# Kernel optimization log

Hardware: AMD Instinct MI355X
Metric: run time of the kernel (lower is better)

Reference implementation:

```python
import jax, jax.numpy as jnp
import numpy as np

B = 65536; T = 7
N_NUM = 32; N_CAT = 16; CARD = 100; D_CAT = 16
D_STATE = 96; D_HID = 192; S_DIM = 64; DT = 1.0
D_IN = N_NUM + N_CAT * D_CAT + 8  # 296
D_Z = 3 * D_STATE + 64            # 352

def _ln(x, g, b, eps=1e-5):
    m = x.mean(-1, keepdims=True)
    v = ((x - m) ** 2).mean(-1, keepdims=True)
    return (x - m) * jax.lax.rsqrt(v + eps) * g + b

def _gelu(x):
    return jax.nn.gelu(x, approximate=False)  # matches torch F.gelu default (erf)

def _forward(x_num, x_static, cat_emb, day_emb, xproj_w, xproj_b, h0,
             bln_g, bln_b, fc1_w, fc1_b, fc2_w, fc2_b,
             spln_g, spln_b, sp1_w, sp1_b, sp2_w, sp2_b,
             base_w, base_b, hln_g, hln_b,
             hm1_w, hm1_b, hm2_w, hm2_b,
             hq1_w, hq1_b, hq2_w, hq2_b,
             hn1_w, hn1_b, hn2_w, hn2_b, x_cat):
    Bsz = x_num.shape[0]
    # categorical embeddings: per-feature table lookup -> (B,T,N_CAT,D_CAT)
    emb = jax.vmap(lambda tab, idx: tab[idx], in_axes=(0, 2), out_axes=2)(cat_emb, x_cat)
    emb = emb.reshape(Bsz, T, N_CAT * D_CAT)
    # day ids are arange(1,8), shared over batch
    day = jnp.broadcast_to(day_emb[1:8], (Bsz, T, 8))
    x = jnp.concatenate([x_num, emb, day], axis=-1)          # (B,T,D_IN)
    x = x @ xproj_w + xproj_b                                # (B,T,D_STATE)

    def step(h, xt):  # Euler-integrated LN+MLP residual cell (dropout = eval identity)
        z = jnp.concatenate([h, xt], axis=-1)                # (B,2*D_STATE)
        z = _ln(z, bln_g, bln_b)
        dh = _gelu(z @ fc1_w + fc1_b) @ fc2_w + fc2_b
        h = h + DT * dh
        return h, h

    h0b = jnp.broadcast_to(h0, (Bsz, D_STATE))
    _, hs = jax.lax.scan(step, h0b, jnp.swapaxes(x, 0, 1))   # (T,B,D_STATE)
    H = jnp.swapaxes(hs, 0, 1)                               # (B,T,D_STATE)
    h_last = H[:, -1]
    h_mean = H.mean(axis=1)
    h_max = H.max(axis=1)

    s = _ln(x_static, spln_g, spln_b)
    s64 = _gelu(s @ sp1_w + sp1_b) @ sp2_w + sp2_b           # (B,64)

    z = jnp.concatenate([h_last, h_mean, h_max, s64], axis=-1)  # (B,D_Z)
    z = _ln(z, hln_g, hln_b)
    base = x_static @ base_w + base_b                        # (B,)
    mean = base + _gelu(z @ hm1_w + hm1_b) @ hm2_w + hm2_b
    q20 = base + _gelu(z @ hq1_w + hq1_b) @ hq2_w + hq2_b
    neg_logit = _gelu(z @ hn1_w + hn1_b) @ hn2_w + hn2_b
    return mean, q20, neg_logit

def setup_inputs() -> dict:
    key = jax.random.key(0)
    ks = iter(jax.random.split(key, 64))
    def w(shape, scale=0.02):
        return (scale * jax.random.normal(next(ks), shape)).astype(jnp.float32)
    def zz(shape):
        return jnp.zeros(shape, jnp.float32)
    def oo(shape):
        return jnp.ones(shape, jnp.float32)
    inp = {
        "x_num": jax.random.normal(next(ks), (B, T, N_NUM), jnp.float32),
        "x_static": jax.random.normal(next(ks), (B, S_DIM), jnp.float32),
        "x_cat": jax.random.randint(next(ks), (B, T, N_CAT), 0, CARD),
        "cat_emb": w((N_CAT, CARD + 1, D_CAT), 1.0),
        "day_emb": w((8, 8), 1.0),
        "xproj_w": w((D_IN, D_STATE)), "xproj_b": zz((D_STATE,)),
        "h0": zz((D_STATE,)),
        "bln_g": oo((2 * D_STATE,)), "bln_b": zz((2 * D_STATE,)),
        "fc1_w": w((2 * D_STATE, D_HID)), "fc1_b": zz((D_HID,)),
        "fc2_w": w((D_HID, D_STATE)), "fc2_b": zz((D_STATE,)),
        "spln_g": oo((S_DIM,)), "spln_b": zz((S_DIM,)),
        "sp1_w": w((S_DIM, 128)), "sp1_b": zz((128,)),
        "sp2_w": w((128, 64)), "sp2_b": zz((64,)),
        "base_w": w((S_DIM,)), "base_b": zz(()),
        "hln_g": oo((D_Z,)), "hln_b": zz((D_Z,)),
        "hm1_w": w((D_Z, D_HID)), "hm1_b": zz((D_HID,)),
        "hm2_w": w((D_HID,)), "hm2_b": zz(()),
        "hq1_w": w((D_Z, D_HID)), "hq1_b": zz((D_HID,)),
        "hq2_w": w((D_HID,)), "hq2_b": zz(()),
        "hn1_w": w((D_Z, D_HID // 2)), "hn1_b": zz((D_HID // 2,)),
        "hn2_w": w((D_HID // 2,)), "hn2_b": zz(()),
    }
    return inp

def reference(x_num, x_static, x_cat, cat_emb, day_emb, xproj_w, xproj_b, h0,
              bln_g, bln_b, fc1_w, fc1_b, fc2_w, fc2_b,
              spln_g, spln_b, sp1_w, sp1_b, sp2_w, sp2_b,
              base_w, base_b, hln_g, hln_b,
              hm1_w, hm1_b, hm2_w, hm2_b,
              hq1_w, hq1_b, hq2_w, hq2_b,
              hn1_w, hn1_b, hn2_w, hn2_b):
    return _forward(x_num, x_static, cat_emb, day_emb, xproj_w, xproj_b, h0,
                    bln_g, bln_b, fc1_w, fc1_b, fc2_w, fc2_b,
                    spln_g, spln_b, sp1_w, sp1_b, sp2_w, sp2_b,
                    base_w, base_b, hln_g, hln_b,
                    hm1_w, hm1_b, hm2_w, hm2_b,
                    hq1_w, hq1_b, hq2_w, hq2_b,
                    hn1_w, hn1_b, hn2_w, hn2_b, x_cat)
```

## Files before the change

kernel.cpp:

```cpp
#include <hip/hip_runtime.h>
#include <math.h>

#define NB 65536

typedef __attribute__((ext_vector_type(8))) short bf16x8;
typedef __attribute__((ext_vector_type(4))) float f32x4;

#define O_BIAST  0
#define O_FC1C   4096
#define O_FC1BP  8192
#define O_FC1FR  12288
#define O_FC2FR  86016
#define O_HDFR   122880
#define O_HDC    460800
#define O_HDBP   462848
#define O_W2C    464896
#define O_SPC    466944
#define O_SPB    467968
#define O_SP1FR  468992
#define O_SP2FR  485376
#define O_XP2FR  501760
#define O_EMB16  557056
#define O_FEAT   608768
#define O_S64    38357504
#define O_STAT   46746112
#define O_BASE   47270400
#define O_XROW   47532544
#define O_XSTAT  135612928

__device__ __forceinline__ unsigned short f2b(float x) {
  unsigned int u = __float_as_uint(x);
  u += 0x7fffu + ((u >> 16) & 1u);
  return (unsigned short)(u >> 16);
}
__device__ __forceinline__ float b2f(unsigned short u) {
  return __uint_as_float(((unsigned)u) << 16);
}
__device__ __forceinline__ float geluf(float x) {
  float z = x * x;
  float e = __builtin_amdgcn_exp2f(-x * (2.3022137f + 0.10294456f * z));
  return x * __builtin_amdgcn_rcpf(1.0f + e);
}

__device__ __forceinline__ void head_fold_part(
    int part, int tid,
    const float* __restrict__ hln_g, const float* __restrict__ hln_b,
    const float* __restrict__ hm1_w, const float* __restrict__ hm1_b,
    const float* __restrict__ hq1_w, const float* __restrict__ hq1_b,
    const float* __restrict__ hn1_w, const float* __restrict__ hn1_b,
    const float* __restrict__ hm2_w, const float* __restrict__ hq2_w,
    const float* __restrict__ hn2_w, char* __restrict__ wsb)
{
  if (tid >= 480) return;
  const int gcol = part*120 + (tid >> 2);
  const int ksl = tid & 3;
  float C = 0.f, Bp = 0.f;
  for (int j = 0; j < 88; ++j) {
    int k = ksl*88 + j;
    float w;
    if (gcol < 192) w = hm1_w[k*192 + gcol];
    else if (gcol < 384) w = hq1_w[k*192 + (gcol-192)];
    else w = hn1_w[k*96 + (gcol-384)];
    C = fmaf(hln_g[k], w, C);
    Bp = fmaf(hln_b[k], w, Bp);
  }
  C += __shfl_xor(C, 1, 64); C += __shfl_xor(C, 2, 64);
  Bp += __shfl_xor(Bp, 1, 64); Bp += __shfl_xor(Bp, 2, 64);
  if (ksl == 0) {
    float b0, w2;
    if (gcol < 192) { b0 = hm1_b[gcol]; w2 = hm2_w[gcol]; }
    else if (gcol < 384) { b0 = hq1_b[gcol-192]; w2 = hq2_w[gcol-192]; }
    else { b0 = hn1_b[gcol-384]; w2 = hn2_w[gcol-384]; }
    ((float*)(wsb + O_HDC))[gcol] = C;
    ((float*)(wsb + O_HDBP))[gcol] = Bp + b0;
    ((float*)(wsb + O_W2C))[gcol] = w2;
  }
}

__global__ void k0_pre(
    const float* __restrict__ cat_emb, const float* __restrict__ day_emb,
    const float* __restrict__ xproj_w, const float* __restrict__ xproj_b,
    const float* __restrict__ bln_g, const float* __restrict__ bln_b,
    const float* __restrict__ fc1_w, const float* __restrict__ fc1_b,
    const float* __restrict__ fc2_w,
    const float* __restrict__ spln_g, const float* __restrict__ spln_b,
    const float* __restrict__ sp1_w, const float* __restrict__ sp1_b,
    const float* __restrict__ sp2_w,
    const float* __restrict__ hln_g, const float* __restrict__ hln_b,
    const float* __restrict__ hm1_w, const float* __restrict__ hm1_b,
    const float* __restrict__ hq1_w, const float* __restrict__ hq1_b,
    const float* __restrict__ hn1_w, const float* __restrict__ hn1_b,
    const float* __restrict__ hm2_w, const float* __restrict__ hq2_w,
    const float* __restrict__ hn2_w,
    char* __restrict__ wsb)
{
  const int b = blockIdx.x, tid = threadIdx.x;
  if (b < 7) {
    if (tid < 96) {
      int t = b;
      float acc = xproj_b[tid];
      #pragma unroll
      for (int d = 0; d < 8; ++d)
        acc = fmaf(day_emb[(1+t)*8 + d], xproj_w[(288+d)*96 + tid], acc);
      ((float*)(wsb + O_BIAST))[t*96 + tid] = acc;
    }
  } else if (b < 9) {
    if (tid < 384) {
      int col = (b-7)*96 + (tid >> 2);
      int ksl = tid & 3;
      float C = 0.f, Bp = 0.f;
      for (int j = 0; j < 48; ++j) {
        int k = ksl*48 + j;
        float w = fc1_w[k*192 + col];
        C = fmaf(bln_g[k], w, C);
        Bp = fmaf(bln_b[k], w, Bp);
      }
      C += __shfl_xor(C, 1, 64); C += __shfl_xor(C, 2, 64);
      Bp += __shfl_xor(Bp, 1, 64); Bp += __shfl_xor(Bp, 2, 64);
      if (ksl == 0) {
        ((float*)(wsb + O_FC1C))[col] = C;
        ((float*)(wsb + O_FC1BP))[col] = Bp + fc1_b[col];
      }
    }
  } else if (b < 81) {
    int seg = b - 9, nt = seg / 6, ks = seg - nt*6;
    int ln = tid >> 3, j = tid & 7;
    int k = ks*32 + (ln>>4)*8 + j, col = nt*16 + (ln&15);
    ((unsigned short*)(wsb + O_FC1FR))[(seg*64 + ln)*8 + j] = f2b(bln_g[k]*fc1_w[k*192 + col]);
  } else if (b < 117) {
    int seg = b - 81, nt = seg / 6, ks = seg - nt*6;
    int ln = tid >> 3, j = tid & 7;
    int k = ks*32 + (ln>>4)*8 + j, col = nt*16 + (ln&15);
    ((unsigned short*)(wsb + O_FC2FR))[(seg*64 + ln)*8 + j] = f2b(fc2_w[k*96 + col]);
  } else if (b < 447) {
    int seg = b - 117, nt = seg / 11, ks = seg - nt*11;
    int ln = tid >> 3, j = tid & 7;
    int k = ks*32 + (ln>>4)*8 + j, gcol = nt*16 + (ln&15);
    float w;
    if (gcol < 192) w = hm1_w[k*192 + gcol];
    else if (gcol < 384) w = hq1_w[k*192 + (gcol-192)];
    else w = hn1_w[k*96 + (gcol-384)];
    ((unsigned short*)(wsb + O_HDFR))[(seg*64 + ln)*8 + j] = f2b(hln_g[k]*w);
  } else if (b < 448) {
    head_fold_part(0, tid, hln_g, hln_b, hm1_w, hm1_b, hq1_w, hq1_b,
                   hn1_w, hn1_b, hm2_w, hq2_w, hn2_w, wsb);
  } else if (b < 449) {
    if (tid < 128) {
      int col = tid;
      float C = 0.f, Bp = sp1_b[col];
      for (int k = 0; k < 64; ++k) {
        float w = sp1_w[k*128 + col];
        C += b2f(f2b(spln_g[k]*w));
        Bp = fmaf(spln_b[k], w, Bp);
      }
      ((float*)(wsb + O_SPC))[col] = C;
      ((float*)(wsb + O_SPB))[col] = Bp;
    }
  } else if (b < 465) {
    int seg = b - 449;
    int ln = tid >> 3, j = tid & 7;
    int nt = seg >> 1, ks = seg & 1;
    int k = ks*32 + (ln>>4)*8 + j, col = nt*16 + (ln&15);
    ((unsigned short*)(wsb + O_SP1FR))[(seg*64 + ln)*8 + j] = f2b(spln_g[k]*sp1_w[k*128 + col]);
  } else if (b < 481) {
    int seg = b - 465;
    int ln = tid >> 3, j = tid & 7;
    int ks = seg & 3;
    int k = ks*32 + (ln>>4)*8 + j, col = (seg >> 2)*16 + (ln&15);
    ((unsigned short*)(wsb + O_SP2FR))[(seg*64 + ln)*8 + j] = f2b(sp2_w[k*64 + col]);
  } else if (b < 535) {
    int seg = b - 481, ks = seg / 6, nt = seg - ks*6;
    int ln = tid >> 3, j = tid & 7;
    int k = ks*32 + (ln>>4)*8 + j, col = nt*16 + (ln&15);
    ((unsigned short*)(wsb + O_XP2FR))[(seg*64 + ln)*8 + j] = f2b(xproj_w[k*96 + col]);
  } else if (b < 586) {
    int i = (b - 535)*512 + tid;
    if (i < 25856)
      ((unsigned short*)(wsb + O_EMB16))[i] = f2b(cat_emb[i]);
  } else {
    head_fold_part(b - 585, tid, hln_g, hln_b, hm1_w, hm1_b, hq1_w, hq1_b,
                   hn1_w, hn1_b, hm2_w, hq2_w, hn2_w, wsb);
  }
}

__global__ __launch_bounds__(256) void k1a_xproj(
    const float* __restrict__ x_num, const int* __restrict__ x_cat,
    const char* __restrict__ wsb, unsigned short* __restrict__ xrow,
    float* __restrict__ xstat)
{
  __shared__ float ctile[4][16][100];
  __shared__ float bsh[7][96];
  const int tid = threadIdx.x;
  const int wv = tid >> 6, l = tid & 63, lr = l & 15, lq = l >> 4;
  const unsigned ctA = blockIdx.x*128u + wv*32u + lr;
  const unsigned ctB = ctA + 16u;
  const int lqh = lq >> 1, lql = lq & 1;

  if (tid < 168)
    ((float4*)bsh)[tid] = ((const float4*)(wsb + O_BIAST))[tid];
  __syncthreads();

  int eA[8], eB[8];
  {
    const int4* ip = (const int4*)(x_cat + (size_t)ctA*16);
    int4 v0 = ip[0], v1 = ip[1], v2 = ip[2], v3 = ip[3];
    eA[0] = lqh ? v0.y : v0.x;  eA[1] = lqh ? v0.w : v0.z;
    eA[2] = lqh ? v1.y : v1.x;  eA[3] = lqh ? v1.w : v1.z;
    eA[4] = lqh ? v2.y : v2.x;  eA[5] = lqh ? v2.w : v2.z;
    eA[6] = lqh ? v3.y : v3.x;  eA[7] = lqh ? v3.w : v3.z;
  }
  {
    const int4* ip = (const int4*)(x_cat + (size_t)ctB*16);
    int4 v0 = ip[0], v1 = ip[1], v2 = ip[2], v3 = ip[3];
    eB[0] = lqh ? v0.y : v0.x;  eB[1] = lqh ? v0.w : v0.z;
    eB[2] = lqh ? v1.y : v1.x;  eB[3] = lqh ? v1.w : v1.z;
    eB[4] = lqh ? v2.y : v2.x;  eB[5] = lqh ? v2.w : v2.z;
    eB[6] = lqh ? v3.y : v3.x;  eB[7] = lqh ? v3.w : v3.z;
  }
  const unsigned short* emb = (const unsigned short*)(wsb + O_EMB16);
  const bf16x8* xp2 = (const bf16x8*)(wsb + O_XP2FR);
  const f32x4 zero4 = {0.f, 0.f, 0.f, 0.f};
  f32x4 accA[6], accB[6];
  #pragma unroll
  for (int nt = 0; nt < 6; ++nt) { accA[nt] = zero4; accB[nt] = zero4; }

  {
    union { bf16x8 v; unsigned short u[8]; } auA, auB;
    {
      const float* xa = x_num + (size_t)ctA*32 + lq*8;
      const float* xb = x_num + (size_t)ctB*32 + lq*8;
      float fa[8], fb[8];
      *(float4*)&fa[0] = *(const float4*)xa;
      *(float4*)&fa[4] = *(const float4*)(xa + 4);
      *(float4*)&fb[0] = *(const float4*)xb;
      *(float4*)&fb[4] = *(const float4*)(xb + 4);
      #pragma unroll
      for (int j = 0; j < 8; ++j) { auA.u[j] = f2b(fa[j]); auB.u[j] = f2b(fb[j]); }
    }
    #pragma unroll
    for (int nt = 0; nt < 6; ++nt) {
      bf16x8 w = xp2[nt*64 + l];
      accA[nt] = __builtin_amdgcn_mfma_f32_16x16x32_bf16(auA.v, w, accA[nt], 0, 0, 0);
      accB[nt] = __builtin_amdgcn_mfma_f32_16x16x32_bf16(auB.v, w, accB[nt], 0, 0, 0);
    }
  }
  #pragma unroll
  for (int c2 = 0; c2 < 8; ++c2) {
    bf16x8 aA = *(const bf16x8*)(emb + ((c2*2+lqh)*101 + eA[c2])*16 + lql*8);
    bf16x8 aB = *(const bf16x8*)(emb + ((c2*2+lqh)*101 + eB[c2])*16 + lql*8);
    #pragma unroll
    for (int nt = 0; nt < 6; ++nt) {
      bf16x8 w = xp2[((c2+1)*6+nt)*64 + l];
      accA[nt] = __builtin_amdgcn_mfma_f32_16x16x32_bf16(aA, w, accA[nt], 0, 0, 0);
      accB[nt] = __builtin_amdgcn_mfma_f32_16x16x32_bf16(aB, w, accB[nt], 0, 0, 0);
    }
  }

  #pragma unroll
  for (int nt = 0; nt < 6; ++nt) {
    #pragma unroll
    for (int i = 0; i < 4; ++i)
      ctile[wv][lq*4 + i][nt*16 + lr] = accA[nt][i];
  }
  asm volatile("s_waitcnt lgkmcnt(0)" ::: "memory");
  __builtin_amdgcn_sched_barrier(0);
  {
    const unsigned t = ctA % 7u;
    float cv[24], bv[24];
    #pragma unroll
    for (int q = 0; q < 6; ++q) {
      *(float4*)&cv[q*4] = *(const float4*)&ctile[wv][lr][lq*24 + q*4];
      *(float4*)&bv[q*4] = *(const float4*)&bsh[t][lq*24 + q*4];
    }
    unsigned ow[12];
    float sm = 0.f, sq = 0.f;
    #pragma unroll
    for (int u = 0; u < 12; ++u) {
      unsigned short u0 = f2b(cv[2*u]   + bv[2*u]);
      unsigned short u1 = f2b(cv[2*u+1] + bv[2*u+1]);
      ow[u] = (unsigned)u0 | ((unsigned)u1 << 16);
      float f0 = b2f(u0), f1 = b2f(u1);
      sm += f0 + f1; sq = fmaf(f0, f0, fmaf(f1, f1, sq));
    }
    {
      uint4* xo = (uint4*)(xrow + (size_t)ctA*96 + lq*24);
      xo[0] = make_uint4(ow[0], ow[1], ow[2], ow[3]);
      xo[1] = make_uint4(ow[4], ow[5], ow[6], ow[7]);
      xo[2] = make_uint4(ow[8], ow[9], ow[10], ow[11]);
    }
    sm += __shfl_xor(sm, 16, 64); sm += __shfl_xor(sm, 32, 64);
    sq += __shfl_xor(sq, 16, 64); sq += __shfl_xor(sq, 32, 64);
    if (lq == 0) {
      float2 o; o.x = sm; o.y = sq;
      *(float2*)(xstat + (size_t)ctA*2) = o;
    }
  }
  asm volatile("s_waitcnt lgkmcnt(0)" ::: "memory");
  __builtin_amdgcn_sched_barrier(0);
  #pragma unroll
  for (int nt = 0; nt < 6; ++nt) {
    #pragma unroll
    for (int i = 0; i < 4; ++i)
      ctile[wv][lq*4 + i][nt*16 + lr] = accB[nt][i];
  }
  asm volatile("s_waitcnt lgkmcnt(0)" ::: "memory");
  __builtin_amdgcn_sched_barrier(0);
  {
    const unsigned t = ctB % 7u;
    float cv[24], bv[24];
    #pragma unroll
    for (int q = 0; q < 6; ++q) {
      *(float4*)&cv[q*4] = *(const float4*)&ctile[wv][lr][lq*24 + q*4];
      *(float4*)&bv[q*4] = *(const float4*)&bsh[t][lq*24 + q*4];
    }
    unsigned ow[12];
    float sm = 0.f, sq = 0.f;
    #pragma unroll
    for (int u = 0; u < 12; ++u) {
      unsigned short u0 = f2b(cv[2*u]   + bv[2*u]);
      unsigned short u1 = f2b(cv[2*u+1] + bv[2*u+1]);
      ow[u] = (unsigned)u0 | ((unsigned)u1 << 16);
      float f0 = b2f(u0), f1 = b2f(u1);
      sm += f0 + f1; sq = fmaf(f0, f0, fmaf(f1, f1, sq));
    }
    {
      uint4* xo = (uint4*)(xrow + (size_t)ctB*96 + lq*24);
      xo[0] = make_uint4(ow[0], ow[1], ow[2], ow[3]);
      xo[1] = make_uint4(ow[4], ow[5], ow[6], ow[7]);
      xo[2] = make_uint4(ow[8], ow[9], ow[10], ow[11]);
    }
    sm += __shfl_xor(sm, 16, 64); sm += __shfl_xor(sm, 32, 64);
    sq += __shfl_xor(sq, 16, 64); sq += __shfl_xor(sq, 32, 64);
    if (lq == 0) {
      float2 o; o.x = sm; o.y = sq;
      *(float2*)(xstat + (size_t)ctB*2) = o;
    }
  }
}

__global__ __launch_bounds__(512, 2) void k1_scan(
    const float* __restrict__ h0, const float* __restrict__ fc2_b,
    const char* __restrict__ wsb, const unsigned short* __restrict__ xrow,
    const float* __restrict__ xstat, unsigned short* __restrict__ feat,
    float* __restrict__ statg)
{
  extern __shared__ char smem[];
  unsigned short* zg = (unsigned short*)smem;
  unsigned short* f1f = (unsigned short*)(smem + 51200);
  unsigned short* f2f = (unsigned short*)(smem + 124928);

  const int tid = threadIdx.x;
  const int wv = tid >> 6;
  const int l = tid & 63;
  const int lr = l & 15;
  const int lq = l >> 4;
  const int rowt = wv*16 + lr;

  {
    const uint4* s1 = (const uint4*)(wsb + O_FC1FR);
    uint4* d1 = (uint4*)f1f;
    for (int o = tid; o < 4608; o += 512) d1[o] = s1[o];
    const uint4* s2 = (const uint4*)(wsb + O_FC2FR);
    uint4* d2 = (uint4*)f2f;
    for (int o = tid; o < 2304; o += 512) d2[o] = s2[o];
  }
  const bf16x8* f1v = (const bf16x8*)f1f;
  const bf16x8* f2v = (const bf16x8*)f2f;

  float C1[12], B1[12];
  {
    const float* fc1C = (const float*)(wsb + O_FC1C);
    const float* fc1BP = (const float*)(wsb + O_FC1BP);
    #pragma unroll
    for (int nt = 0; nt < 12; ++nt) { C1[nt] = fc1C[nt*16+lr]; B1[nt] = fc1BP[nt*16+lr]; }
  }
  float fb2[6];
  #pragma unroll
  for (int nt = 0; nt < 6; ++nt) fb2[nt] = fc2_b[nt*16+lr];

  float h[24], hs[24], hm[24];
  #pragma unroll
  for (int nt = 0; nt < 6; ++nt) {
    float v = h0[nt*16+lr];
    #pragma unroll
    for (int i = 0; i < 4; ++i) { h[nt*4+i] = v; hs[nt*4+i] = 0.f; hm[nt*4+i] = -3.4e38f; }
  }
  __syncthreads();

  const f32x4 zero4 = {0.f, 0.f, 0.f, 0.f};
  const size_t srow_q = (size_t)blockIdx.x*128 + wv*16;

  for (int t = 0; t < 7; ++t) {
    float hsm[4] = {0.f,0.f,0.f,0.f}, hsq[4] = {0.f,0.f,0.f,0.f};
    #pragma unroll
    for (int nt = 0; nt < 6; ++nt) {
      #pragma unroll
      for (int i = 0; i < 4; ++i) {
        unsigned short hb = f2b(h[nt*4+i]);
        zg[(wv*16 + lq*4 + i)*200 + nt*16 + lr] = hb;
        float hf = b2f(hb);
        hsm[i] += hf; hsq[i] = fmaf(hf, hf, hsq[i]);
      }
    }
    #pragma unroll
    for (int i = 0; i < 4; ++i) {
      hsm[i] += __shfl_xor(hsm[i], 1, 64); hsm[i] += __shfl_xor(hsm[i], 2, 64);
      hsm[i] += __shfl_xor(hsm[i], 4, 64); hsm[i] += __shfl_xor(hsm[i], 8, 64);
      hsq[i] += __shfl_xor(hsq[i], 1, 64); hsq[i] += __shfl_xor(hsq[i], 2, 64);
      hsq[i] += __shfl_xor(hsq[i], 4, 64); hsq[i] += __shfl_xor(hsq[i], 8, 64);
    }
    float mr[4], rr[4];
    #pragma unroll
    for (int i = 0; i < 4; ++i) {
      const float2 xs = *(const float2*)(xstat + ((srow_q + lq*4 + i)*7 + t)*2);
      float m = (hsm[i] + xs.x) * (1.f/192.f);
      float var = (hsq[i] + xs.y) * (1.f/192.f) - m*m;
      mr[i] = m; rr[i] = rsqrtf(var + 1e-5f);
    }
    bf16x8 ax[3];
    {
      const unsigned short* xp = xrow + ((srow_q + lr)*7 + t)*96;
      #pragma unroll
      for (int k3 = 0; k3 < 3; ++k3)
        ax[k3] = *(const bf16x8*)(xp + k3*32 + lq*8);
    }
    f32x4 acc[12];
    #pragma unroll
    for (int nt = 0; nt < 12; ++nt) acc[nt] = zero4;
    #pragma unroll
    for (int ks = 0; ks < 3; ++ks) {
      bf16x8 a = *(const bf16x8*)(zg + rowt*200 + ks*32 + lq*8);
      #pragma unroll
      for (int nt = 0; nt < 12; ++nt)
        acc[nt] = __builtin_amdgcn_mfma_f32_16x16x32_bf16(a, f1v[(nt*6+ks)*64 + l], acc[nt], 0, 0, 0);
    }
    #pragma unroll
    for (int k3 = 0; k3 < 3; ++k3) {
      #pragma unroll
      for (int nt = 0; nt < 12; ++nt)
        acc[nt] = __builtin_amdgcn_mfma_f32_16x16x32_bf16(ax[k3], f1v[(nt*6+k3+3)*64 + l], acc[nt], 0, 0, 0);
    }
    #pragma unroll
    for (int nt = 0; nt < 12; ++nt) {
      #pragma unroll
      for (int i = 0; i < 4; ++i) {
        float hid = rr[i]*(acc[nt][i] - mr[i]*C1[nt]) + B1[nt];
        zg[(wv*16 + lq*4 + i)*200 + nt*16 + lr] = f2b(geluf(hid));
      }
    }
    f32x4 a2[6];
    #pragma unroll
    for (int nt = 0; nt < 6; ++nt) a2[nt] = zero4;
    #pragma unroll
    for (int ks = 0; ks < 6; ++ks) {
      bf16x8 a = *(const bf16x8*)(zg + rowt*200 + ks*32 + lq*8);
      #pragma unroll
      for (int nt = 0; nt < 6; ++nt)
        a2[nt] = __builtin_amdgcn_mfma_f32_16x16x32_bf16(a, f2v[(nt*6+ks)*64 + l], a2[nt], 0, 0, 0);
    }
    #pragma unroll
    for (int nt = 0; nt < 6; ++nt) {
      #pragma unroll
      for (int i = 0; i < 4; ++i) {
        int u = nt*4 + i;
        h[u] += a2[nt][i] + fb2[nt];
        hs[u] += h[u];
        hm[u] = fmaxf(hm[u], h[u]);
      }
    }
  }
  float st[4] = {0.f,0.f,0.f,0.f}, qt[4] = {0.f,0.f,0.f,0.f};
  #pragma unroll
  for (int nt = 0; nt < 6; ++nt) {
    #pragma unroll
    for (int i = 0; i < 4; ++i) {
      size_t r = (srow_q + lq*4 + i)*288;
      int c = nt*16 + lr;
      unsigned short b0 = f2b(h[nt*4+i]);
      unsigned short b1 = f2b(hs[nt*4+i]*(1.f/7.f));
      unsigned short b2v = f2b(hm[nt*4+i]);
      feat[r + c] = b0;
      feat[r + 96 + c] = b1;
      feat[r + 192 + c] = b2v;
      float f0 = b2f(b0), f1 = b2f(b1), f2v = b2f(b2v);
      st[i] += f0 + f1 + f2v;
      qt[i] = fmaf(f0, f0, fmaf(f1, f1, fmaf(f2v, f2v, qt[i])));
    }
  }
  #pragma unroll
  for (int i = 0; i < 4; ++i) {
    st[i] += __shfl_xor(st[i], 1, 64); st[i] += __shfl_xor(st[i], 2, 64);
    st[i] += __shfl_xor(st[i], 4, 64); st[i] += __shfl_xor(st[i], 8, 64);
    qt[i] += __shfl_xor(qt[i], 1, 64); qt[i] += __shfl_xor(qt[i], 2, 64);
    qt[i] += __shfl_xor(qt[i], 4, 64); qt[i] += __shfl_xor(qt[i], 8, 64);
  }
  if (lr == 0) {
    #pragma unroll
    for (int i = 0; i < 4; ++i) {
      size_t r = srow_q + lq*4 + i;
      float2 o; o.x = st[i]; o.y = qt[i];
      *(float2*)(statg + r*2) = o;
    }
  }
}

__global__ __launch_bounds__(512, 2) void k1b_static(
    const float* __restrict__ x_static, const float* __restrict__ sp2_b,
    const float* __restrict__ base_w, const float* __restrict__ base_b,
    char* __restrict__ wsb)
{
  __shared__ char smem[68608];
  unsigned short* sp1f = (unsigned short*)smem;
  unsigned short* sp2f = (unsigned short*)(smem + 16384);
  unsigned short* hid  = (unsigned short*)(smem + 32768);

  const int tid = threadIdx.x;
  const int wv = tid >> 6, l = tid & 63, lr = l & 15, lq = l >> 4;
  const int srow = blockIdx.x*128 + wv*16;

  {
    const uint4* s1 = (const uint4*)(wsb + O_SP1FR);
    uint4* d1 = (uint4*)sp1f;
    for (int o = tid; o < 1024; o += 512) d1[o] = s1[o];
    const uint4* s2 = (const uint4*)(wsb + O_SP2FR);
    uint4* d2 = (uint4*)sp2f;
    for (int o = tid; o < 1024; o += 512) d2[o] = s2[o];
  }
  __syncthreads();

  float x0f[8], x1f[8];
  {
    const float* xr = x_static + (size_t)(srow + lr)*64;
    *(float4*)&x0f[0] = *(const float4*)(xr + lq*8);
    *(float4*)&x0f[4] = *(const float4*)(xr + lq*8 + 4);
    *(float4*)&x1f[0] = *(const float4*)(xr + 32 + lq*8);
    *(float4*)&x1f[4] = *(const float4*)(xr + 32 + lq*8 + 4);
  }
  float sm = 0.f, sq = 0.f, bp = 0.f;
  #pragma unroll
  for (int j = 0; j < 8; ++j) {
    sm += x0f[j] + x1f[j];
    sq = fmaf(x0f[j], x0f[j], fmaf(x1f[j], x1f[j], sq));
    bp = fmaf(x0f[j], base_w[lq*8 + j], fmaf(x1f[j], base_w[32 + lq*8 + j], bp));
  }
  sm += __shfl_xor(sm, 16, 64); sm += __shfl_xor(sm, 32, 64);
  sq += __shfl_xor(sq, 16, 64); sq += __shfl_xor(sq, 32, 64);
  bp += __shfl_xor(bp, 16, 64); bp += __shfl_xor(bp, 32, 64);
  if (lq == 0) ((float*)(wsb + O_BASE))[srow + lr] = bp + base_b[0];
  const float ms = sm*(1.f/64.f);
  const float rs = rsqrtf(sq*(1.f/64.f) - ms*ms + 1e-5f);
  float mr[4], rr[4];
  #pragma unroll
  for (int i = 0; i < 4; ++i) {
    mr[i] = __shfl(ms, lq*4 + i, 16);
    rr[i] = __shfl(rs, lq*4 + i, 16);
  }
  union { bf16x8 v; unsigned short u[8]; } ua0, ua1;
  #pragma unroll
  for (int j = 0; j < 8; ++j) { ua0.u[j] = f2b(x0f[j]); ua1.u[j] = f2b(x1f[j]); }

  const f32x4 zero4 = {0.f, 0.f, 0.f, 0.f};
  const bf16x8* f1 = (const bf16x8*)sp1f;
  const bf16x8* f2 = (const bf16x8*)sp2f;
  unsigned short* hw = hid + wv*2176;

  f32x4 acc[8];
  #pragma unroll
  for (int nt = 0; nt < 8; ++nt) acc[nt] = zero4;
  #pragma unroll
  for (int nt = 0; nt < 8; ++nt) {
    acc[nt] = __builtin_amdgcn_mfma_f32_16x16x32_bf16(ua0.v, f1[(nt*2 + 0)*64 + l], acc[nt], 0, 0, 0);
    acc[nt] = __builtin_amdgcn_mfma_f32_16x16x32_bf16(ua1.v, f1[(nt*2 + 1)*64 + l], acc[nt], 0, 0, 0);
  }
  {
    const float* spC = (const float*)(wsb + O_SPC);
    const float* spB = (const float*)(wsb + O_SPB);
    #pragma unroll
    for (int nt = 0; nt < 8; ++nt) {
      float Cv = spC[nt*16 + lr], Bv = spB[nt*16 + lr];
      #pragma unroll
      for (int i = 0; i < 4; ++i) {
        float hv = rr[i]*(acc[nt][i] - mr[i]*Cv) + Bv;
        hw[(lq*4 + i)*136 + nt*16 + lr] = f2b(geluf(hv));
      }
    }
  }
  f32x4 a2[4];
  #pragma unroll
  for (int nt = 0; nt < 4; ++nt) a2[nt] = zero4;
  #pragma unroll
  for (int ks = 0; ks < 4; ++ks) {
    bf16x8 a = *(const bf16x8*)(hw + lr*136 + ks*32 + lq*8);
    #pragma unroll
    for (int nt = 0; nt < 4; ++nt)
      a2[nt] = __builtin_amdgcn_mfma_f32_16x16x32_bf16(a, f2[(nt*4 + ks)*64 + l], a2[nt], 0, 0, 0);
  }
  float ss[4] = {0.f,0.f,0.f,0.f}, qq[4] = {0.f,0.f,0.f,0.f};
  {
    unsigned short* s64p = (unsigned short*)(wsb + O_S64);
    #pragma unroll
    for (int nt = 0; nt < 4; ++nt) {
      float bv = sp2_b[nt*16 + lr];
      #pragma unroll
      for (int i = 0; i < 4; ++i) {
        unsigned short rb = f2b(a2[nt][i] + bv);
        s64p[(size_t)(srow + lq*4 + i)*64 + nt*16 + lr] = rb;
        float f = b2f(rb);
        ss[i] += f; qq[i] = fmaf(f, f, qq[i]);
      }
    }
  }
  #pragma unroll
  for (int i = 0; i < 4; ++i) {
    ss[i] += __shfl_xor(ss[i], 1, 64); ss[i] += __shfl_xor(ss[i], 2, 64);
    ss[i] += __shfl_xor(ss[i], 4, 64); ss[i] += __shfl_xor(ss[i], 8, 64);
    qq[i] += __shfl_xor(qq[i], 1, 64); qq[i] += __shfl_xor(qq[i], 2, 64);
    qq[i] += __shfl_xor(qq[i], 4, 64); qq[i] += __shfl_xor(qq[i], 8, 64);
  }
  if (lr == 0) {
    float* stat = (float*)(wsb + O_STAT);
    #pragma unroll
    for (int i = 0; i < 4; ++i) {
      size_t r = (size_t)srow + lq*4 + i;
      float2 fs = *(float2*)(stat + r*2);
      float stot = fs.x + ss[i], qtot = fs.y + qq[i];
      float m = stot*(1.f/352.f);
      float var = qtot*(1.f/352.f) - m*m;
      float2 o; o.x = m; o.y = rsqrtf(var + 1e-5f);
      *(float2*)(stat + r*2) = o;
    }
  }
}

__global__ __launch_bounds__(512, 2) void k2b_heads(
    const float* __restrict__ hm2_b, const float* __restrict__ hq2_b,
    const float* __restrict__ hn2_b, const char* __restrict__ wsb,
    const unsigned short* __restrict__ feat, float* __restrict__ out)
{
  extern __shared__ char smem[];
  const int g = blockIdx.y;
  const int tid = threadIdx.x;
  const int wv = tid >> 6, l = tid & 63, lr = l & 15, lq = l >> 4;
  const int ntn = (g == 2) ? 6 : 12;
  {
    const uint4* src = (const uint4*)(wsb + O_HDFR + (size_t)g*135168);
    uint4* dst = (uint4*)smem;
    const int n = ntn*11*64;
    for (int o = tid; o < n; o += 512) dst[o] = src[o];
  }
  __syncthreads();
  const bf16x8* wfr = (const bf16x8*)smem;
  const float* hdC = (const float*)(wsb + O_HDC);
  const float* hdB = (const float*)(wsb + O_HDBP);
  const float* w2c = (const float*)(wsb + O_W2C);
  const float* stat = (const float*)(wsb + O_STAT);
  const float* baseb = (const float*)(wsb + O_BASE);
  const unsigned short* s64p = (const unsigned short*)(wsb + O_S64);
  const float hb = (g == 0) ? hm2_b[0] : (g == 1) ? hq2_b[0] : hn2_b[0];
  const f32x4 zero4 = {0.f, 0.f, 0.f, 0.f};

  for (int c = blockIdx.x; c < 256; c += gridDim.x) {
    const int base = c*256 + wv*32;
    bf16x8 afr0[11], afr1[11];
    {
      const unsigned short* fr0 = feat + (size_t)(base + lr)*288;
      const unsigned short* fr1 = feat + (size_t)(base + 16 + lr)*288;
      #pragma unroll
      for (int ks = 0; ks < 9; ++ks) {
        afr0[ks] = *(const bf16x8*)(fr0 + ks*32 + lq*8);
        afr1[ks] = *(const bf16x8*)(fr1 + ks*32 + lq*8);
      }
      const unsigned short* sr0 = s64p + (size_t)(base + lr)*64;
      const unsigned short* sr1 = s64p + (size_t)(base + 16 + lr)*64;
      afr0[9]  = *(const bf16x8*)(sr0 + lq*8);
      afr0[10] = *(const bf16x8*)(sr0 + 32 + lq*8);
      afr1[9]  = *(const bf16x8*)(sr1 + lq*8);
      afr1[10] = *(const bf16x8*)(sr1 + 32 + lq*8);
    }
    float mr0[4], rr0[4], mr1[4], rr1[4];
    #pragma unroll
    for (int i = 0; i < 4; ++i) {
      float2 s0 = *(const float2*)(stat + (size_t)(base + lq*4 + i)*2);
      float2 s1 = *(const float2*)(stat + (size_t)(base + 16 + lq*4 + i)*2);
      mr0[i] = s0.x; rr0[i] = s0.y; mr1[i] = s1.x; rr1[i] = s1.y;
    }
    float pr0[4] = {0.f,0.f,0.f,0.f}, pr1[4] = {0.f,0.f,0.f,0.f};
    for (int nt = 0; nt < ntn; ++nt) {
      const int col = (g*12 + nt)*16 + lr;
      const float Cv = hdC[col], Bv = hdB[col], w2v = w2c[col];
      f32x4 a0 = zero4, a1v = zero4;
      #pragma unroll
      for (int ks = 0; ks < 11; ++ks) {
        bf16x8 b = wfr[(nt*11 + ks)*64 + l];
        a0  = __builtin_amdgcn_mfma_f32_16x16x32_bf16(afr0[ks], b, a0, 0, 0, 0);
        a1v = __builtin_amdgcn_mfma_f32_16x16x32_bf16(afr1[ks], b, a1v, 0, 0, 0);
      }
      #pragma unroll
      for (int i = 0; i < 4; ++i) {
        pr0[i] += geluf(rr0[i]*(a0[i]  - mr0[i]*Cv) + Bv) * w2v;
        pr1[i] += geluf(rr1[i]*(a1v[i] - mr1[i]*Cv) + Bv) * w2v;
      }
    }
    #pragma unroll
    for (int i = 0; i < 4; ++i) {
      float v0 = pr0[i], v1 = pr1[i];
      v0 += __shfl_xor(v0, 1, 64); v0 += __shfl_xor(v0, 2, 64);
      v0 += __shfl_xor(v0, 4, 64); v0 += __shfl_xor(v0, 8, 64);
      v1 += __shfl_xor(v1, 1, 64); v1 += __shfl_xor(v1, 2, 64);
      v1 += __shfl_xor(v1, 4, 64); v1 += __shfl_xor(v1, 8, 64);
      if (lr == 0) {
        int r0 = base + lq*4 + i;
        int r1 = base + 16 + lq*4 + i;
        float b0 = (g < 2) ? baseb[r0] : 0.f;
        float b1 = (g < 2) ? baseb[r1] : 0.f;
        out[(size_t)g*NB + r0] = b0 + hb + v0;
        out[(size_t)g*NB + r1] = b1 + hb + v1;
      }
    }
  }
}

extern "C" void kernel_launch(void* const* d_in, const int* in_sizes, int n_in,
                              void* d_out, int out_size, void* d_ws, size_t ws_size,
                              hipStream_t stream) {
  (void)in_sizes; (void)n_in; (void)out_size; (void)ws_size;
  const float* x_num    = (const float*)d_in[0];
  const float* x_static = (const float*)d_in[1];
  const int*   x_cat    = (const int*)  d_in[2];
  const float* cat_emb  = (const float*)d_in[3];
  const float* day_emb  = (const float*)d_in[4];
  const float* xproj_w  = (const float*)d_in[5];
  const float* xproj_b  = (const float*)d_in[6];
  const float* h0       = (const float*)d_in[7];
  const float* bln_g    = (const float*)d_in[8];
  const float* bln_b    = (const float*)d_in[9];
  const float* fc1_w    = (const float*)d_in[10];
  const float* fc1_b    = (const float*)d_in[11];
  const float* fc2_w    = (const float*)d_in[12];
  const float* fc2_b    = (const float*)d_in[13];
  const float* spln_g   = (const float*)d_in[14];
  const float* spln_b   = (const float*)d_in[15];
  const float* sp1_w    = (const float*)d_in[16];
  const float* sp1_b    = (const float*)d_in[17];
  const float* sp2_w    = (const float*)d_in[18];
  const float* sp2_b    = (const float*)d_in[19];
  const float* base_w   = (const float*)d_in[20];
  const float* base_b   = (const float*)d_in[21];
  const float* hln_g    = (const float*)d_in[22];
  const float* hln_b    = (const float*)d_in[23];
  const float* hm1_w    = (const float*)d_in[24];
  const float* hm1_b    = (const float*)d_in[25];
  const float* hm2_w    = (const float*)d_in[26];
  const float* hm2_b    = (const float*)d_in[27];
  const float* hq1_w    = (const float*)d_in[28];
  const float* hq1_b    = (const float*)d_in[29];
  const float* hq2_w    = (const float*)d_in[30];
  const float* hq2_b    = (const float*)d_in[31];
  const float* hn1_w    = (const float*)d_in[32];
  const float* hn1_b    = (const float*)d_in[33];
  const float* hn2_w    = (const float*)d_in[34];
  const float* hn2_b    = (const float*)d_in[35];

  char* wsb = (char*)d_ws;
  unsigned short* feat = (unsigned short*)(wsb + O_FEAT);
  unsigned short* xrow = (unsigned short*)(wsb + O_XROW);
  float* xstat = (float*)(wsb + O_XSTAT);
  float* statg = (float*)(wsb + O_STAT);
  float* out = (float*)d_out;

  k0_pre<<<589, 512, 0, stream>>>(cat_emb, day_emb, xproj_w, xproj_b,
      bln_g, bln_b, fc1_w, fc1_b, fc2_w, spln_g, spln_b, sp1_w, sp1_b, sp2_w,
      hln_g, hln_b, hm1_w, hm1_b, hq1_w, hq1_b, hn1_w, hn1_b,
      hm2_w, hq2_w, hn2_w, wsb);
  k1a_xproj<<<3584, 256, 0, stream>>>(x_num, x_cat, wsb, xrow, xstat);
  k1_scan<<<512, 512, 161792, stream>>>(h0, fc2_b, wsb, xrow, xstat, feat, statg);
  k1b_static<<<512, 512, 0, stream>>>(x_static, sp2_b, base_w, base_b, wsb);
  k2b_heads<<<dim3(64, 3), 512, 135168, stream>>>(hm2_b, hq2_b, hn2_b,
      wsb, feat, out);
}
```

Before: 284.3 us.

## Fold static-MLP kernel into xproj kernel via extra blocks and reorder stat finalization

The separate static-feature MLP kernel is merged into the xproj kernel as 1024 extra 256-thread blocks that run alongside the xproj blocks. It now writes partial row sums, and the scan kernel reads those and finalizes the head LayerNorm statistics. This removes one launch and lets the static work overlap the xproj work instead of running after the scan. The static path now reads its MLP weight fragments straight from global memory instead of staging them in shared memory. The shared buffer also shrinks to fit the smaller xproj tile.

```diff
diff --git a/kernel.cpp b/kernel.cpp
--- a/kernel.cpp
+++ b/kernel.cpp
@@ -183,15 +183,124 @@
   }
 }
 
-__global__ __launch_bounds__(256) void k1a_xproj(
+__global__ __launch_bounds__(256) void k1ab(
     const float* __restrict__ x_num, const int* __restrict__ x_cat,
-    const char* __restrict__ wsb, unsigned short* __restrict__ xrow,
+    const float* __restrict__ x_static, const float* __restrict__ sp2_b,
+    const float* __restrict__ base_w, const float* __restrict__ base_b,
+    char* __restrict__ wsb, unsigned short* __restrict__ xrow,
     float* __restrict__ xstat)
 {
-  __shared__ float ctile[4][16][100];
-  __shared__ float bsh[7][96];
+  __shared__ char smem[28288];
   const int tid = threadIdx.x;
   const int wv = tid >> 6, l = tid & 63, lr = l & 15, lq = l >> 4;
+  const f32x4 zero4 = {0.f, 0.f, 0.f, 0.f};
+
+  if (blockIdx.x >= 3584) {
+    unsigned short* hid = (unsigned short*)smem;
+    const int srow = (blockIdx.x - 3584)*64 + wv*16;
+
+    float x0f[8], x1f[8];
+    {
+      const float* xr = x_static + (size_t)(srow + lr)*64;
+      *(float4*)&x0f[0] = *(const float4*)(xr + lq*8);
+      *(float4*)&x0f[4] = *(const float4*)(xr + lq*8 + 4);
+      *(float4*)&x1f[0] = *(const float4*)(xr + 32 + lq*8);
+      *(float4*)&x1f[4] = *(const float4*)(xr + 32 + lq*8 + 4);
+    }
+    float sm = 0.f, sq = 0.f, bp = 0.f;
+    #pragma unroll
+    for (int j = 0; j < 8; ++j) {
+      sm += x0f[j] + x1f[j];
+      sq = fmaf(x0f[j], x0f[j], fmaf(x1f[j], x1f[j], sq));
+      bp = fmaf(x0f[j], base_w[lq*8 + j], fmaf(x1f[j], base_w[32 + lq*8 + j], bp));
+    }
+    sm += __shfl_xor(sm, 16, 64); sm += __shfl_xor(sm, 32, 64);
+    sq += __shfl_xor(sq, 16, 64); sq += __shfl_xor(sq, 32, 64);
+    bp += __shfl_xor(bp, 16, 64); bp += __shfl_xor(bp, 32, 64);
+    if (lq == 0) ((float*)(wsb + O_BASE))[srow + lr] = bp + base_b[0];
+    const float ms = sm*(1.f/64.f);
+    const float rs = rsqrtf(sq*(1.f/64.f) - ms*ms + 1e-5f);
+    float mr[4], rr[4];
+    #pragma unroll
+    for (int i = 0; i < 4; ++i) {
+      mr[i] = __shfl(ms, lq*4 + i, 16);
+      rr[i] = __shfl(rs, lq*4 + i, 16);
+    }
+    union { bf16x8 v; unsigned short u[8]; } ua0, ua1;
+    #pragma unroll
+    for (int j = 0; j < 8; ++j) { ua0.u[j] = f2b(x0f[j]); ua1.u[j] = f2b(x1f[j]); }
+
+    const bf16x8* f1 = (const bf16x8*)(wsb + O_SP1FR);
+    const bf16x8* f2 = (const bf16x8*)(wsb + O_SP2FR);
+    unsigned short* hw = hid + wv*2176;
+
+    f32x4 acc[8];
+    #pragma unroll
+    for (int nt = 0; nt < 8; ++nt) acc[nt] = zero4;
+    #pragma unroll
+    for (int nt = 0; nt < 8; ++nt) {
+      acc[nt] = __builtin_amdgcn_mfma_f32_16x16x32_bf16(ua0.v, f1[(nt*2 + 0)*64 + l], acc[nt], 0, 0, 0);
+      acc[nt] = __builtin_amdgcn_mfma_f32_16x16x32_bf16(ua1.v, f1[(nt*2 + 1)*64 + l], acc[nt], 0, 0, 0);
+    }
+    {
+      const float* spC = (const float*)(wsb + O_SPC);
+      const float* spB = (const float*)(wsb + O_SPB);
+      #pragma unroll
+      for (int nt = 0; nt < 8; ++nt) {
+        float Cv = spC[nt*16 + lr], Bv = spB[nt*16 + lr];
+        #pragma unroll
+        for (int i = 0; i < 4; ++i) {
+          float hv = rr[i]*(acc[nt][i] - mr[i]*Cv) + Bv;
+          hw[(lq*4 + i)*136 + nt*16 + lr] = f2b(geluf(hv));
+        }
+      }
+    }
+    f32x4 a2[4];
+    #pragma unroll
+    for (int nt = 0; nt < 4; ++nt) a2[nt] = zero4;
+    #pragma unroll
+    for (int ks = 0; ks < 4; ++ks) {
+      bf16x8 a = *(const bf16x8*)(hw + lr*136 + ks*32 + lq*8);
+      #pragma unroll
+      for (int nt = 0; nt < 4; ++nt)
+        a2[nt] = __builtin_amdgcn_mfma_f32_16x16x32_bf16(a, f2[(nt*4 + ks)*64 + l], a2[nt], 0, 0, 0);
+    }
+    float ss[4] = {0.f,0.f,0.f,0.f}, qq[4] = {0.f,0.f,0.f,0.f};
+    {
+      unsigned short* s64p = (unsigned short*)(wsb + O_S64);
+      #pragma unroll
+      for (int nt = 0; nt < 4; ++nt) {
+        float bv = sp2_b[nt*16 + lr];
+        #pragma unroll
+        for (int i = 0; i < 4; ++i) {
+          unsigned short rb = f2b(a2[nt][i] + bv);
+          s64p[(size_t)(srow + lq*4 + i)*64 + nt*16 + lr] = rb;
+          float f = b2f(rb);
+          ss[i] += f; qq[i] = fmaf(f, f, qq[i]);
+        }
+      }
+    }
+    #pragma unroll
+    for (int i = 0; i < 4; ++i) {
+      ss[i] += __shfl_xor(ss[i], 1, 64); ss[i] += __shfl_xor(ss[i], 2, 64);
+      ss[i] += __shfl_xor(ss[i], 4, 64); ss[i] += __shfl_xor(ss[i], 8, 64);
+      qq[i] += __shfl_xor(qq[i], 1, 64); qq[i] += __shfl_xor(qq[i], 2, 64);
+      qq[i] += __shfl_xor(qq[i], 4, 64); qq[i] += __shfl_xor(qq[i], 8, 64);
+    }
+    if (lr == 0) {
+      float* stat = (float*)(wsb + O_STAT);
+      #pragma unroll
+      for (int i = 0; i < 4; ++i) {
+        size_t r = (size_t)srow + lq*4 + i;
+        float2 o; o.x = ss[i]; o.y = qq[i];
+        *(float2*)(stat + r*2) = o;
+      }
+    }
+    return;
+  }
+
+  float (*ctile)[16][100] = (float(*)[16][100])smem;
+  float (*bsh)[96] = (float(*)[96])(smem + 25600);
   const unsigned ctA = blockIdx.x*128u + wv*32u + lr;
   const unsigned ctB = ctA + 16u;
   const int lqh = lq >> 1, lql = lq & 1;
@@ -219,7 +328,6 @@
   }
   const unsigned short* emb = (const unsigned short*)(wsb + O_EMB16);
   const bf16x8* xp2 = (const bf16x8*)(wsb + O_XP2FR);
-  const f32x4 zero4 = {0.f, 0.f, 0.f, 0.f};
   f32x4 accA[6], accB[6];
   #pragma unroll
   for (int nt = 0; nt < 6; ++nt) { accA[nt] = zero4; accB[nt] = zero4; }
@@ -498,136 +606,12 @@
     #pragma unroll
     for (int i = 0; i < 4; ++i) {
       size_t r = srow_q + lq*4 + i;
-      float2 o; o.x = st[i]; o.y = qt[i];
-      *(float2*)(statg + r*2) = o;
-    }
-  }
-}
-
-__global__ __launch_bounds__(512, 2) void k1b_static(
-    const float* __restrict__ x_static, const float* __restrict__ sp2_b,
-    const float* __restrict__ base_w, const float* __restrict__ base_b,
-    char* __restrict__ wsb)
-{
-  __shared__ char smem[68608];
-  unsigned short* sp1f = (unsigned short*)smem;
-  unsigned short* sp2f = (unsigned short*)(smem + 16384);
-  unsigned short* hid  = (unsigned short*)(smem + 32768);
-
-  const int tid = threadIdx.x;
-  const int wv = tid >> 6, l = tid & 63, lr = l & 15, lq = l >> 4;
-  const int srow = blockIdx.x*128 + wv*16;
-
-  {
-    const uint4* s1 = (const uint4*)(wsb + O_SP1FR);
-    uint4* d1 = (uint4*)sp1f;
-    for (int o = tid; o < 1024; o += 512) d1[o] = s1[o];
-    const uint4* s2 = (const uint4*)(wsb + O_SP2FR);
-    uint4* d2 = (uint4*)sp2f;
-    for (int o = tid; o < 1024; o += 512) d2[o] = s2[o];
-  }
-  __syncthreads();
-
-  float x0f[8], x1f[8];
-  {
-    const float* xr = x_static + (size_t)(srow + lr)*64;
-    *(float4*)&x0f[0] = *(const float4*)(xr + lq*8);
-    *(float4*)&x0f[4] = *(const float4*)(xr + lq*8 + 4);
-    *(float4*)&x1f[0] = *(const float4*)(xr + 32 + lq*8);
-    *(float4*)&x1f[4] = *(const float4*)(xr + 32 + lq*8 + 4);
-  }
-  float sm = 0.f, sq = 0.f, bp = 0.f;
-  #pragma unroll
-  for (int j = 0; j < 8; ++j) {
-    sm += x0f[j] + x1f[j];
-    sq = fmaf(x0f[j], x0f[j], fmaf(x1f[j], x1f[j], sq));
-    bp = fmaf(x0f[j], base_w[lq*8 + j], fmaf(x1f[j], base_w[32 + lq*8 + j], bp));
-  }
-  sm += __shfl_xor(sm, 16, 64); sm += __shfl_xor(sm, 32, 64);
-  sq += __shfl_xor(sq, 16, 64); sq += __shfl_xor(sq, 32, 64);
-  bp += __shfl_xor(bp, 16, 64); bp += __shfl_xor(bp, 32, 64);
-  if (lq == 0) ((float*)(wsb + O_BASE))[srow + lr] = bp + base_b[0];
-  const float ms = sm*(1.f/64.f);
-  const float rs = rsqrtf(sq*(1.f/64.f) - ms*ms + 1e-5f);
-  float mr[4], rr[4];
-  #pragma unroll
-  for (int i = 0; i < 4; ++i) {
-    mr[i] = __shfl(ms, lq*4 + i, 16);
-    rr[i] = __shfl(rs, lq*4 + i, 16);
-  }
-  union { bf16x8 v; unsigned short u[8]; } ua0, ua1;
-  #pragma unroll
-  for (int j = 0; j < 8; ++j) { ua0.u[j] = f2b(x0f[j]); ua1.u[j] = f2b(x1f[j]); }
-
-  const f32x4 zero4 = {0.f, 0.f, 0.f, 0.f};
-  const bf16x8* f1 = (const bf16x8*)sp1f;
-  const bf16x8* f2 = (const bf16x8*)sp2f;
-  unsigned short* hw = hid + wv*2176;
-
-  f32x4 acc[8];
-  #pragma unroll
-  for (int nt = 0; nt < 8; ++nt) acc[nt] = zero4;
-  #pragma unroll
-  for (int nt = 0; nt < 8; ++nt) {
-    acc[nt] = __builtin_amdgcn_mfma_f32_16x16x32_bf16(ua0.v, f1[(nt*2 + 0)*64 + l], acc[nt], 0, 0, 0);
-    acc[nt] = __builtin_amdgcn_mfma_f32_16x16x32_bf16(ua1.v, f1[(nt*2 + 1)*64 + l], acc[nt], 0, 0, 0);
-  }
-  {
-    const float* spC = (const float*)(wsb + O_SPC);
-    const float* spB = (const float*)(wsb + O_SPB);
-    #pragma unroll
-    for (int nt = 0; nt < 8; ++nt) {
-      float Cv = spC[nt*16 + lr], Bv = spB[nt*16 + lr];
-      #pragma unroll
-      for (int i = 0; i < 4; ++i) {
-        float hv = rr[i]*(acc[nt][i] - mr[i]*Cv) + Bv;
-        hw[(lq*4 + i)*136 + nt*16 + lr] = f2b(geluf(hv));
-      }
-    }
-  }
-  f32x4 a2[4];
-  #pragma unroll
-  for (int nt = 0; nt < 4; ++nt) a2[nt] = zero4;
-  #pragma unroll
-  for (int ks = 0; ks < 4; ++ks) {
-    bf16x8 a = *(const bf16x8*)(hw + lr*136 + ks*32 + lq*8);
-    #pragma unroll
-    for (int nt = 0; nt < 4; ++nt)
-      a2[nt] = __builtin_amdgcn_mfma_f32_16x16x32_bf16(a, f2[(nt*4 + ks)*64 + l], a2[nt], 0, 0, 0);
-  }
-  float ss[4] = {0.f,0.f,0.f,0.f}, qq[4] = {0.f,0.f,0.f,0.f};
-  {
-    unsigned short* s64p = (unsigned short*)(wsb + O_S64);
-    #pragma unroll
-    for (int nt = 0; nt < 4; ++nt) {
-      float bv = sp2_b[nt*16 + lr];
-      #pragma unroll
-      for (int i = 0; i < 4; ++i) {
-        unsigned short rb = f2b(a2[nt][i] + bv);
-        s64p[(size_t)(srow + lq*4 + i)*64 + nt*16 + lr] = rb;
-        float f = b2f(rb);
-        ss[i] += f; qq[i] = fmaf(f, f, qq[i]);
-      }
-    }
-  }
-  #pragma unroll
-  for (int i = 0; i < 4; ++i) {
-    ss[i] += __shfl_xor(ss[i], 1, 64); ss[i] += __shfl_xor(ss[i], 2, 64);
-    ss[i] += __shfl_xor(ss[i], 4, 64); ss[i] += __shfl_xor(ss[i], 8, 64);
-    qq[i] += __shfl_xor(qq[i], 1, 64); qq[i] += __shfl_xor(qq[i], 2, 64);
-    qq[i] += __shfl_xor(qq[i], 4, 64); qq[i] += __shfl_xor(qq[i], 8, 64);
-  }
-  if (lr == 0) {
-    float* stat = (float*)(wsb + O_STAT);
-    #pragma unroll
-    for (int i = 0; i < 4; ++i) {
-      size_t r = (size_t)srow + lq*4 + i;
-      float2 fs = *(float2*)(stat + r*2);
-      float stot = fs.x + ss[i], qtot = fs.y + qq[i];
+      float2 fs = *(float2*)(statg + r*2);
+      float stot = fs.x + st[i], qtot = fs.y + qt[i];
       float m = stot*(1.f/352.f);
       float var = qtot*(1.f/352.f) - m*m;
       float2 o; o.x = m; o.y = rsqrtf(var + 1e-5f);
-      *(float2*)(stat + r*2) = o;
+      *(float2*)(statg + r*2) = o;
     }
   }
 }
@@ -772,9 +756,9 @@
       bln_g, bln_b, fc1_w, fc1_b, fc2_w, spln_g, spln_b, sp1_w, sp1_b, sp2_w,
       hln_g, hln_b, hm1_w, hm1_b, hq1_w, hq1_b, hn1_w, hn1_b,
       hm2_w, hq2_w, hn2_w, wsb);
-  k1a_xproj<<<3584, 256, 0, stream>>>(x_num, x_cat, wsb, xrow, xstat);
+  k1ab<<<4608, 256, 0, stream>>>(x_num, x_cat, x_static, sp2_b, base_w, base_b,
+      wsb, xrow, xstat);
   k1_scan<<<512, 512, 161792, stream>>>(h0, fc2_b, wsb, xrow, xstat, feat, statg);
-  k1b_static<<<512, 512, 0, stream>>>(x_static, sp2_b, base_w, base_b, wsb);
   k2b_heads<<<dim3(64, 3), 512, 135168, stream>>>(hm2_b, hq2_b, hn2_b,
       wsb, feat, out);
 }
```

Result: faster. 278.6 us, median of 2 (-2.0%).
